# Performance work log

Measured on AMD Instinct MI355X. Metric: run time of the kernel, lower is better.

The kernel has to match this reference:

```python
import jax, jax.numpy as jnp
import numpy as np

NUM_MATCHES = 10
ALPHA = 0.75
INV_COEFF = 25.0
VAR_COEFF = 15.0
COV_COEFF = 1.0
GAMMA = 1.0


def cdist(a, b):
    # Euclidean pairwise distances via the matmul form (as torch.cdist p=2 does).
    d2 = (jnp.sum(a * a, -1)[:, :, None] + jnp.sum(b * b, -1)[:, None, :]
          - 2.0 * jnp.einsum('bnd,bmd->bnm', a, b))
    return jnp.sqrt(jnp.maximum(d2, 0.0))


def nearest_neighbors(input_maps, candidate_maps, distances, k):
    # Indices are constants wrt grads in the original (topk values discarded).
    distances = jax.lax.stop_gradient(distances)
    nn_d = jnp.min(distances, axis=-1)       # [B, N] distance to closest candidate
    nn_i = jnp.argmin(distances, axis=-1)    # [B, N] index of closest candidate
    _, element_indices = jax.lax.top_k(-nn_d, k)  # k elements with smallest NN distance
    candidate_indices = jnp.take_along_axis(nn_i, element_indices, axis=-1)
    # FAITHFUL to the source: torch gather with index shape [B, k, 1] keeps ONLY
    # feature channel 0 -> filtered maps have shape [B, k, 1].
    fi = jnp.take_along_axis(input_maps[:, :, :1], element_indices[:, :, None], axis=1)
    fc = jnp.take_along_axis(candidate_maps[:, :, :1], candidate_indices[:, :, None], axis=1)
    return fi, fc


def local_variance_loss(x, gamma):
    x = x - jnp.mean(x, axis=1, keepdims=True)
    std = jnp.sqrt(jnp.var(x, axis=1, ddof=1))  # torch std: unbiased
    return jnp.mean(jax.nn.relu(gamma - std))


def local_covariance_loss(x):
    B, N, D = x.shape
    x = x - jnp.mean(x, axis=1, keepdims=True)
    cov = jnp.einsum('bnd,bne->bde', x, x) / (N - 1)
    off_diag = 1.0 - jnp.eye(D, dtype=x.dtype)
    return jnp.sum((cov * off_diag) ** 2) / (D * B)


def local_vicreg_loss(x, y):
    inv = INV_COEFF * jnp.mean((x - y) ** 2)
    var = VAR_COEFF * (local_variance_loss(x, GAMMA) + local_variance_loss(y, GAMMA)) / 2
    cov = COV_COEFF * (local_covariance_loss(x) + local_covariance_loss(y)) / 2
    return inv, var, cov, inv + var + cov


def global_vicreg_loss(x, y):
    inv = INV_COEFF * jnp.mean((x - y) ** 2)

    def var_loss(z):
        std = jnp.sqrt(jnp.var(z, axis=0, ddof=1))
        return jnp.mean(jax.nn.relu(GAMMA - std))

    def cov_loss(z):
        n, d = z.shape
        z = z - jnp.mean(z, axis=0)
        cov = (z.T @ z) / (n - 1)
        off = 1.0 - jnp.eye(d, dtype=z.dtype)
        return jnp.sum((cov * off) ** 2) / d

    var = VAR_COEFF * (var_loss(x) + var_loss(y)) / 2
    cov = COV_COEFF * (cov_loss(x) + cov_loss(y)) / 2
    return inv, var, cov, inv + var + cov


def vicregl_forward(x1_maps, x2_maps, x1_glob, x2_glob, x1_locations, x2_locations):
    g = global_vicreg_loss(x1_glob, x2_glob)

    def location_loss(im, cm, il, cl):
        fi, fc = nearest_neighbors(im, cm, cdist(il, cl), NUM_MATCHES)
        return local_vicreg_loss(fi, fc)

    def feature_loss(im, cm):
        fi, fc = nearest_neighbors(im, cm, cdist(im, cm), NUM_MATCHES)
        return local_vicreg_loss(fi, fc)

    l1 = location_loss(x1_maps, x2_maps, x1_locations, x2_locations)
    l2 = location_loss(x2_maps, x1_maps, x2_locations, x1_locations)
    loc = tuple((a + b) / 2 for a, b in zip(l1, l2))

    f1 = feature_loss(x1_maps, x2_maps)
    f2 = feature_loss(x2_maps, x1_maps)
    feat = tuple((a + b) / 2 for a, b in zip(f1, f2))

    total = ALPHA * g[3] + (1.0 - ALPHA) * (feat[3] + loc[3]) / 2
    # Order: loss, global/(inv,var,cov,loss), location/(...), feature/(...)
    return jnp.stack([total, *g, *loc, *feat])


def setup_inputs() -> dict:
    key = jax.random.key(0)
    ks = jax.random.split(key, 6)
    B, N, D, G = 64, 1024, 512, 8192
    return {
        'x1_maps': jax.random.normal(ks[0], (B, N, D), jnp.float32),
        'x2_maps': jax.random.normal(ks[1], (B, N, D), jnp.float32),
        'x1_glob': jax.random.normal(ks[2], (B, G), jnp.float32),
        'x2_glob': jax.random.normal(ks[3], (B, G), jnp.float32),
        'x1_locations': jax.random.uniform(ks[4], (B, N, 2), jnp.float32),
        'x2_locations': jax.random.uniform(ks[5], (B, N, 2), jnp.float32),
    }


def reference(x1_maps, x2_maps, x1_glob, x2_glob, x1_locations, x2_locations):
    return vicregl_forward(x1_maps, x2_maps, x1_glob, x2_glob, x1_locations, x2_locations)
```

## Files before the change

kernel.cpp:

```cpp
#include <hip/hip_runtime.h>
#include <math.h>

#define NB 64
#define NN 1024
#define ND 512
#define NG 8192
#define FINF __builtin_inff()

typedef unsigned short u16;
typedef unsigned int   u32;
typedef short  short8 __attribute__((ext_vector_type(8)));
typedef float  f32x4  __attribute__((ext_vector_type(4)));

static const size_t OFF_AHL = 0;
static const size_t OFF_BHL = 33554432ull;
static const size_t PBASE_FAST = 67108864ull;

static const size_t OFF_FRPV = 0;
static const size_t OFF_FRPI = 524288;
static const size_t OFF_FCPV = 1048576;
static const size_t OFF_FCPI = 1572864;
static const size_t OFF_FRV  = 2097152;
static const size_t OFF_FRI  = 2162688;
static const size_t OFF_FCV  = 2228224;
static const size_t OFF_FCI  = 2293760;
static const size_t OFF_LRV  = 2359296;
static const size_t OFF_LRI  = 2424832;
static const size_t OFF_LCV  = 2490368;
static const size_t OFF_LCI  = 2555904;
static const size_t OFF_GP   = 2621440;
static const size_t OFF_SCAL = 3670016;
static const size_t OFF_SEL  = 3671056;
static const size_t OFF_RA   = 3676176;
static const size_t OFF_RB   = 3741712;
static const size_t OFF_GRED = 3807248;
static const size_t PBLOCK_END = 3807312;

__device__ __forceinline__ void upd(float& bv, int& bi, float v, int i){
  if (v < bv || (v == bv && i < bi)) { bv = v; bi = i; }
}

__device__ __forceinline__ u16 f2bf(float x){
  u32 u = __float_as_uint(x);
  u32 r = u + 0x7FFFu + ((u >> 16) & 1u);
  return (u16)(r >> 16);
}
__device__ __forceinline__ float bf2f(u16 h){ return __uint_as_float(((u32)h) << 16); }

__global__ __launch_bounds__(256) void convert_kernel(
    const float* __restrict__ X, u16* __restrict__ HL, float* __restrict__ norms)
{
  const int wid = threadIdx.x >> 6, lane = threadIdx.x & 63;
  const size_t row = (size_t)blockIdx.x * 4 + wid;
  const float* src = X + row * ND + lane * 8;
  float4 v0 = *(const float4*)src;
  float4 v1 = *(const float4*)(src + 4);
  float xs[8] = {v0.x, v0.y, v0.z, v0.w, v1.x, v1.y, v1.z, v1.w};
  short8 hi, lo;
  float nrm = 0.f;
  #pragma unroll
  for (int k = 0; k < 8; k++){
    u16 h = f2bf(xs[k]);
    float hf = bf2f(h);
    u16 l = f2bf(xs[k] - hf);
    hi[k] = (short)h; lo[k] = (short)l;
    nrm = fmaf(xs[k], xs[k], nrm);
  }
  #pragma unroll
  for (int off = 1; off < 64; off <<= 1) nrm += __shfl_xor(nrm, off);
  *(short8*)(HL + row * 1024 + lane * 8)       = hi;
  *(short8*)(HL + row * 1024 + 512 + lane * 8) = lo;
  if (lane == 0) norms[row] = nrm;
}

__device__ __forceinline__ int akoff(int s){ int p = s >> 3; return ((p == 2) ? 512 : 0) + (s & 7) * 64; }
__device__ __forceinline__ int bkoff(int s){ int p = s >> 3; return ((p == 1) ? 512 : 0) + (s & 7) * 64; }

__global__ __launch_bounds__(256) void feat_mfma_kernel(
    const u16* __restrict__ Ahl, const u16* __restrict__ Bhl,
    const float* __restrict__ ran, const float* __restrict__ rbn,
    float* __restrict__ rp_v, int* __restrict__ rp_i,
    float* __restrict__ cp_v, int* __restrict__ cp_i)
{
  const int blk = blockIdx.x;
  const int wg  = (blk & 7) * 512 + (blk >> 3);
  const int b = wg >> 6, t64 = wg & 63;
  const int ns = t64 >> 3, mt = t64 & 7;

  __shared__ u16 As[128 * 64];
  __shared__ u16 Bs[128 * 64];
  __shared__ float ra_s[128], rb_s[128];
  __shared__ float rowv[2][128]; __shared__ int rowi[2][128];
  __shared__ float colv[2][128]; __shared__ int coli[2][128];

  const int t = threadIdx.x;
  const int lane = t & 63, wid = t >> 6;
  const int wr = wid >> 1, wc = wid & 1;
  const int R0 = wr * 64, C0 = wc * 64;
  const int g4 = lane >> 4, l15 = lane & 15, swz = lane & 7;

  const u16* Agrow = Ahl + ((size_t)b * 1024 + ns * 128) * 1024;
  const u16* Bgrow = Bhl + ((size_t)b * 1024 + mt * 128) * 1024;

  if (t < 128) ra_s[t]       = ran[(size_t)b * 1024 + ns * 128 + t];
  else         rb_s[t - 128] = rbn[(size_t)b * 1024 + mt * 128 + (t - 128)];

  f32x4 acc[4][4];
  #pragma unroll
  for (int i = 0; i < 4; i++)
    #pragma unroll
    for (int j = 0; j < 4; j++){ f32x4 z = {0.f, 0.f, 0.f, 0.f}; acc[i][j] = z; }

  auto stage = [&](const u16* grow, u16* lds, int koff){
    #pragma unroll
    for (int i2 = 0; i2 < 4; i2++){
      int c = i2 * 256 + t;
      int row = c >> 3, col16 = c & 7;
      int srcc = col16 ^ (row & 7);
      const u16* g = grow + (size_t)row * 1024 + koff + srcc * 8;
      __builtin_amdgcn_global_load_lds(
          (const __attribute__((address_space(1))) void*)g,
          (__attribute__((address_space(3))) void*)(lds + c * 8),
          16, 0, 0);
    }
  };

  stage(Agrow, As, akoff(0));
  stage(Bgrow, Bs, bkoff(0));

  for (int s = 0; s < 24; s++){
    __syncthreads();
    #pragma unroll
    for (int kk = 0; kk < 64; kk += 32){
      short8 af[4], bfv[4];
      #pragma unroll
      for (int i2 = 0; i2 < 4; i2++){
        int ac16 = ((kk >> 3) + g4) ^ swz;
        int ar = R0 + i2 * 16 + l15;
        af[i2]  = *(const short8*)&As[ar * 64 + ac16 * 8];
        int br = C0 + i2 * 16 + l15;
        bfv[i2] = *(const short8*)&Bs[br * 64 + ac16 * 8];
      }
      #pragma unroll
      for (int i2 = 0; i2 < 4; i2++)
        #pragma unroll
        for (int j2 = 0; j2 < 4; j2++)
          acc[i2][j2] = __builtin_amdgcn_mfma_f32_16x16x32_bf16(af[i2], bfv[j2], acc[i2][j2], 0, 0, 0);
    }
    __syncthreads();
    if (s < 23){
      stage(Agrow, As, akoff(s + 1));
      stage(Bgrow, Bs, bkoff(s + 1));
    }
  }

  #pragma unroll
  for (int i2 = 0; i2 < 4; i2++){
    #pragma unroll
    for (int reg = 0; reg < 4; reg++){
      int rloc = R0 + i2 * 16 + g4 * 4 + reg;
      float rav = ra_s[rloc];
      float bv = FINF; int bi = 0;
      #pragma unroll
      for (int j2 = 0; j2 < 4; j2++){
        float d2 = rav + rb_s[C0 + j2 * 16 + l15] - 2.f * acc[i2][j2][reg];
        upd(bv, bi, d2, mt * 128 + C0 + j2 * 16 + l15);
      }
      #pragma unroll
      for (int off = 1; off < 16; off <<= 1){
        float ov = __shfl_xor(bv, off);
        int   oi = __shfl_xor(bi, off);
        upd(bv, bi, ov, oi);
      }
      if (l15 == 0){ rowv[wc][rloc] = bv; rowi[wc][rloc] = bi; }
    }
  }
  #pragma unroll
  for (int j2 = 0; j2 < 4; j2++){
    int cloc = C0 + j2 * 16 + l15;
    float rbv = rb_s[cloc];
    float bv = FINF; int bi = 0;
    #pragma unroll
    for (int i2 = 0; i2 < 4; i2++)
      #pragma unroll
      for (int reg = 0; reg < 4; reg++){
        float d2 = ra_s[R0 + i2 * 16 + g4 * 4 + reg] + rbv - 2.f * acc[i2][j2][reg];
        upd(bv, bi, d2, ns * 128 + R0 + i2 * 16 + g4 * 4 + reg);
      }
    #pragma unroll
    for (int off = 16; off < 64; off <<= 1){
      float ov = __shfl_xor(bv, off);
      int   oi = __shfl_xor(bi, off);
      upd(bv, bi, ov, oi);
    }
    if (g4 == 0){ colv[wr][cloc] = bv; coli[wr][cloc] = bi; }
  }
  __syncthreads();
  if (t < 128){
    float bv = rowv[0][t]; int bi = rowi[0][t];
    upd(bv, bi, rowv[1][t], rowi[1][t]);
    size_t o = ((size_t)b * 8 + mt) * NN + ns * 128 + t;
    rp_v[o] = bv; rp_i[o] = bi;
  } else {
    int c2 = t - 128;
    float bv = colv[0][c2]; int bi = coli[0][c2];
    upd(bv, bi, colv[1][c2], coli[1][c2]);
    size_t o = ((size_t)b * 8 + ns) * NN + mt * 128 + c2;
    cp_v[o] = bv; cp_i[o] = bi;
  }
}

__global__ __launch_bounds__(256) void feat_tile_kernel(
    const float* __restrict__ A, const float* __restrict__ Bm,
    float* __restrict__ rp_v, int* __restrict__ rp_i,
    float* __restrict__ cp_v, int* __restrict__ cp_i)
{
  const int blk = blockIdx.x;
  const int mt = blk & 7, ns = (blk >> 3) & 7, b = blk >> 6;
  const float* __restrict__ Ab = A  + ((size_t)b*NN + ns*128)*ND;
  const float* __restrict__ Bb = Bm + ((size_t)b*NN + mt*128)*ND;

  __shared__ __align__(16) float As[32*132];
  __shared__ __align__(16) float Bs[32*132];
  __shared__ float rasum[128], rbsum[128];
  __shared__ float colv[16*128];
  __shared__ int   coli[16*128];

  const int t = threadIdx.x;
  const int tx = t & 15, ty = t >> 4;

  float acc[8][8];
  #pragma unroll
  for (int i=0;i<8;i++)
    #pragma unroll
    for (int j=0;j<8;j++) acc[i][j]=0.f;
  float ra_acc=0.f, rb_acc=0.f;

  for (int kt=0; kt<ND; kt+=32){
    #pragma unroll
    for (int i=0;i<4;i++){
      int q = t + i*256;
      int r = q >> 3, f4 = q & 7;
      const float4 av  = *(const float4*)(Ab + (size_t)r*ND + kt + f4*4);
      const float4 bv4 = *(const float4*)(Bb + (size_t)r*ND + kt + f4*4);
      int kk = f4*4;
      As[(kk+0)*132+r]=av.x;  As[(kk+1)*132+r]=av.y;  As[(kk+2)*132+r]=av.z;  As[(kk+3)*132+r]=av.w;
      Bs[(kk+0)*132+r]=bv4.x; Bs[(kk+1)*132+r]=bv4.y; Bs[(kk+2)*132+r]=bv4.z; Bs[(kk+3)*132+r]=bv4.w;
    }
    __syncthreads();
    if (t < 128){
      #pragma unroll
      for (int kk=0;kk<32;kk++){ float v=As[kk*132+t]; ra_acc = fmaf(v,v,ra_acc); }
    } else {
      int c = t-128;
      #pragma unroll
      for (int kk=0;kk<32;kk++){ float v=Bs[kk*132+c]; rb_acc = fmaf(v,v,rb_acc); }
    }
    #pragma unroll
    for (int kk=0;kk<32;kk++){
      float a0[8], b0[8];
      *(float4*)&a0[0] = *(const float4*)&As[kk*132 + ty*8];
      *(float4*)&a0[4] = *(const float4*)&As[kk*132 + ty*8 + 4];
      *(float4*)&b0[0] = *(const float4*)&Bs[kk*132 + tx*8];
      *(float4*)&b0[4] = *(const float4*)&Bs[kk*132 + tx*8 + 4];
      #pragma unroll
      for (int i=0;i<8;i++)
        #pragma unroll
        for (int j=0;j<8;j++)
          acc[i][j] = fmaf(a0[i], b0[j], acc[i][j]);
    }
    __syncthreads();
  }

  if (t<128) rasum[t]=ra_acc; else rbsum[t-128]=rb_acc;
  __syncthreads();

  float ra[8], rb[8];
  #pragma unroll
  for (int i=0;i<8;i++){ ra[i]=rasum[ty*8+i]; rb[i]=rbsum[tx*8+i]; }

  const int n0g = ns*128, m0g = mt*128;

  #pragma unroll
  for (int i=0;i<8;i++){
    float bv = FINF; int bi = 0;
    #pragma unroll
    for (int j=0;j<8;j++){
      float d2 = ra[i] + rb[j] - 2.f*acc[i][j];
      upd(bv, bi, d2, m0g + tx*8 + j);
    }
    #pragma unroll
    for (int off=1; off<16; off<<=1){
      float ov = __shfl_xor(bv, off);
      int   oi = __shfl_xor(bi, off);
      upd(bv, bi, ov, oi);
    }
    if (tx==0){
      size_t o = ((size_t)b*8 + mt)*NN + n0g + ty*8 + i;
      rp_v[o] = bv; rp_i[o] = bi;
    }
  }
  #pragma unroll
  for (int j=0;j<8;j++){
    float bv = FINF; int bi = 0;
    #pragma unroll
    for (int i=0;i<8;i++){
      float d2 = ra[i] + rb[j] - 2.f*acc[i][j];
      upd(bv, bi, d2, n0g + ty*8 + i);
    }
    colv[ty*128 + tx*8 + j] = bv;
    coli[ty*128 + tx*8 + j] = bi;
  }
  __syncthreads();
  if (t < 128){
    float bv = FINF; int bi = 0;
    for (int y2=0;y2<16;y2++) upd(bv, bi, colv[y2*128+t], coli[y2*128+t]);
    size_t o = ((size_t)b*8 + ns)*NN + m0g + t;
    cp_v[o]=bv; cp_i[o]=bi;
  }
}

__global__ __launch_bounds__(256) void merge_kernel(
    const float* __restrict__ rp_v, const int* __restrict__ rp_i,
    const float* __restrict__ cp_v, const int* __restrict__ cp_i,
    float* __restrict__ row_v, int* __restrict__ row_i,
    float* __restrict__ col_v, int* __restrict__ col_i)
{
  int tid = blockIdx.x*256 + threadIdx.x;
  int which = tid >> 16;
  int r = tid & 65535;
  int b = r >> 10, n = r & 1023;
  float bv = FINF; int bi = 0;
  if (which == 0){
    #pragma unroll
    for (int p=0;p<8;p++){
      size_t o = ((size_t)b*8+p)*NN + n;
      upd(bv,bi, rp_v[o], rp_i[o]);
    }
    row_v[(size_t)b*NN+n]=bv; row_i[(size_t)b*NN+n]=bi;
  } else {
    #pragma unroll
    for (int p=0;p<8;p++){
      size_t o = ((size_t)b*8+p)*NN + n;
      upd(bv,bi, cp_v[o], cp_i[o]);
    }
    col_v[(size_t)b*NN+n]=bv; col_i[(size_t)b*NN+n]=bi;
  }
}

__global__ __launch_bounds__(256) void loc_kernel(
    const float* __restrict__ L1, const float* __restrict__ L2,
    float* __restrict__ lr_v, int* __restrict__ lr_i,
    float* __restrict__ lc_v, int* __restrict__ lc_i)
{
  int b = blockIdx.x >> 2, part = blockIdx.x & 3, t = threadIdx.x;
  __shared__ float2 p1[NN], p2[NN];
  for (int i=t;i<NN;i+=256){
    p1[i] = ((const float2*)L1)[(size_t)b*NN+i];
    p2[i] = ((const float2*)L2)[(size_t)b*NN+i];
  }
  __syncthreads();
  int n = part*256 + t;
  {
    float2 a = p1[n];
    float bv=FINF; int bi=0;
    for (int m=0;m<NN;m++){
      float dx=a.x-p2[m].x, dy=a.y-p2[m].y;
      float d2 = dx*dx+dy*dy;
      if (d2 < bv){ bv=d2; bi=m; }
    }
    lr_v[(size_t)b*NN+n]=bv; lr_i[(size_t)b*NN+n]=bi;
  }
  {
    float2 a = p2[n];
    float bv=FINF; int bi=0;
    for (int q=0;q<NN;q++){
      float dx=a.x-p1[q].x, dy=a.y-p1[q].y;
      float d2 = dx*dx+dy*dy;
      if (d2 < bv){ bv=d2; bi=q; }
    }
    lc_v[(size_t)b*NN+n]=bv; lc_i[(size_t)b*NN+n]=bi;
  }
}

__global__ __launch_bounds__(256) void glob_part_kernel(
    const float* __restrict__ X, const float* __restrict__ Y,
    float* __restrict__ Gpart, float* __restrict__ scalpart)
{
  int blk = blockIdx.x, t = threadIdx.x;
  int d0 = blk*64;
  __shared__ float xt[64*65];
  __shared__ float yt[64*65];
  __shared__ float red[256];

  float inv_part = 0.f;
  #pragma unroll
  for (int i=0;i<16;i++){
    int q = t + i*256;
    int n = q>>6, c = q&63;
    float xv = X[(size_t)n*NG + d0 + c];
    float yv = Y[(size_t)n*NG + d0 + c];
    xt[n*65+c]=xv; yt[n*65+c]=yv;
    float df = xv-yv; inv_part += df*df;
  }
  __syncthreads();

  float relu_part=0.f, csq2_part=0.f;
  if (t < 128){
    int c = t & 63;
    float* Z = (t<64)? xt : yt;
    float s=0.f;
    for (int n=0;n<64;n++) s += Z[n*65+c];
    float mu = s*(1.f/64.f);
    float sq=0.f;
    for (int n=0;n<64;n++){ float v=Z[n*65+c]-mu; Z[n*65+c]=v; sq = fmaf(v,v,sq); }
    float sd = sqrtf(sq*(1.f/63.f));
    relu_part = fmaxf(0.f, 1.f-sd);
    csq2_part = sq*sq;
  }
  __syncthreads();

  int ti=(t>>4)*4, tj=(t&15)*4;
  for (int pass=0; pass<2; pass++){
    const float* Z = pass? yt : xt;
    float g[4][4] = {};
    for (int c=0;c<64;c++){
      float vi[4], vj[4];
      #pragma unroll
      for (int k2=0;k2<4;k2++){ vi[k2]=Z[(ti+k2)*65+c]; vj[k2]=Z[(tj+k2)*65+c]; }
      #pragma unroll
      for (int a2=0;a2<4;a2++)
        #pragma unroll
        for (int b2=0;b2<4;b2++) g[a2][b2] = fmaf(vi[a2], vj[b2], g[a2][b2]);
    }
    float* gp = Gpart + ((size_t)blk*2+pass)*4096;
    #pragma unroll
    for (int a2=0;a2<4;a2++)
      #pragma unroll
      for (int b2=0;b2<4;b2++) gp[(ti+a2)*64 + tj + b2] = g[a2][b2];
  }

  auto bsum = [&](float v)->float{
    red[t]=v; __syncthreads();
    for (int s=128;s;s>>=1){ if (t<s) red[t]+=red[t+s]; __syncthreads(); }
    float r=red[0]; __syncthreads(); return r;
  };
  float inv_s = bsum(inv_part);
  float rx_s  = bsum(t<64 ? relu_part : 0.f);
  float ry_s  = bsum((t>=64 && t<128)? relu_part : 0.f);
  float cx_s  = bsum(t<64 ? csq2_part : 0.f);
  float cy_s  = bsum((t>=64 && t<128)? csq2_part : 0.f);
  if (t==0){
    float* sp = scalpart + blk*8;
    sp[0]=inv_s; sp[1]=rx_s; sp[2]=ry_s; sp[3]=cx_s; sp[4]=cy_s;
  }
}

__global__ __launch_bounds__(256) void glob_reduce2_kernel(
    const float* __restrict__ Gpart, float* __restrict__ gred)
{
  int g = blockIdx.x, t = threadIdx.x;
  __shared__ float red[256];
  int pass = t >> 7, e = g*128 + (t & 127);
  float s = 0.f;
  for (int blk=0; blk<128; blk++) s += Gpart[((size_t)blk*2 + pass)*4096 + e];
  red[t] = s*s; __syncthreads();
  for (int st=64; st; st>>=1){ if ((t&127) < st) red[t] += red[t+st]; __syncthreads(); }
  if ((t&127)==0) gred[g*2 + pass] = red[t];
}

__global__ __launch_bounds__(64) void select_kernel(
    const float* __restrict__ x1m, const float* __restrict__ x2m,
    const float* __restrict__ frv, const int* __restrict__ fri,
    const float* __restrict__ fcv, const int* __restrict__ fci,
    const float* __restrict__ lrv, const int* __restrict__ lri,
    const float* __restrict__ lcv, const int* __restrict__ lci,
    float* __restrict__ selout)
{
  int sel = blockIdx.x >> 6, b = blockIdx.x & 63;
  const float* nnv; const int* nni; const float* inm; const float* cnm;
  if      (sel==0){ nnv=frv; nni=fri; inm=x1m; cnm=x2m; }
  else if (sel==1){ nnv=fcv; nni=fci; inm=x2m; cnm=x1m; }
  else if (sel==2){ nnv=lrv; nni=lri; inm=x1m; cnm=x2m; }
  else            { nnv=lcv; nni=lci; inm=x2m; cnm=x1m; }

  int lane = threadIdx.x;
  float v[16];
  #pragma unroll
  for (int j=0;j<16;j++) v[j] = nnv[(size_t)b*NN + j*64 + lane];
  __shared__ int wins[10];
  for (int it=0; it<10; it++){
    float bv = FINF; int bi = 0x7fffffff;
    #pragma unroll
    for (int j=0;j<16;j++) upd(bv, bi, v[j], j*64+lane);
    #pragma unroll
    for (int off=1; off<64; off<<=1){
      float ov = __shfl_xor(bv, off);
      int   oi = __shfl_xor(bi, off);
      upd(bv, bi, ov, oi);
    }
    #pragma unroll
    for (int j=0;j<16;j++) if (j*64+lane == bi) v[j] = FINF;
    if (lane==0) wins[it] = bi;
  }
  __syncthreads();
  if (lane < 10){
    int e = wins[lane];
    int c = nni[(size_t)b*NN + e];
    float fi = inm[((size_t)b*NN + e)*ND];
    float fc = cnm[((size_t)b*NN + c)*ND];
    float2* so = (float2*)selout;
    so[((size_t)sel*64 + b)*10 + lane] = make_float2(fi, fc);
  }
}

__global__ __launch_bounds__(64) void final_kernel(
    const float* __restrict__ selout, const float* __restrict__ gred,
    const float* __restrict__ scalpart, float* __restrict__ out)
{
  int lane = threadIdx.x;
  float ssx = (lane<32)? gred[lane*2]   : 0.f;
  float ssy = (lane<32)? gred[lane*2+1] : 0.f;
  const float* sp0 = scalpart + (size_t)lane*8;
  const float* sp1 = scalpart + (size_t)(lane+64)*8;
  float inv_p = sp0[0]+sp1[0];
  float rx = sp0[1]+sp1[1], ry = sp0[2]+sp1[2];
  float cx = sp0[3]+sp1[3], cy = sp0[4]+sp1[4];
  #pragma unroll
  for (int off=1; off<64; off<<=1){
    ssx += __shfl_xor(ssx,off); ssy += __shfl_xor(ssy,off);
    inv_p += __shfl_xor(inv_p,off);
    rx += __shfl_xor(rx,off); ry += __shfl_xor(ry,off);
    cx += __shfl_xor(cx,off); cy += __shfl_xor(cy,off);
  }

  float inv_s[4], var_s[4];
  #pragma unroll
  for (int sel=0; sel<4; sel++){
    const float2* so = (const float2*)selout + ((size_t)sel*64 + lane)*10;
    float x[10], y[10];
    float sx=0.f, sy=0.f, sd2=0.f;
    #pragma unroll
    for (int j=0;j<10;j++){
      float2 p = so[j];
      x[j]=p.x; y[j]=p.y;
      sx+=p.x; sy+=p.y;
      float d=p.x-p.y; sd2 = fmaf(d,d,sd2);
    }
    float mx = sx*0.1f, my = sy*0.1f;
    float vx=0.f, vy=0.f;
    #pragma unroll
    for (int j=0;j<10;j++){
      float dx=x[j]-mx, dy=y[j]-my;
      vx = fmaf(dx,dx,vx); vy = fmaf(dy,dy,vy);
    }
    vx *= (1.f/9.f); vy *= (1.f/9.f);
    float rvx = fmaxf(0.f, 1.f - sqrtf(vx));
    float rvy = fmaxf(0.f, 1.f - sqrtf(vy));
    float a=sd2, b2=rvx, c=rvy;
    #pragma unroll
    for (int off=32; off; off>>=1){
      a  += __shfl_xor(a, off);
      b2 += __shfl_xor(b2, off);
      c  += __shfl_xor(c, off);
    }
    inv_s[sel] = 25.f * a * (1.f/640.f);
    var_s[sel] = 15.f*0.5f*(b2*(1.f/64.f) + c*(1.f/64.f));
  }
  if (lane==0){
    float g_inv = 25.f * inv_p / (64.f*8192.f);
    float g_var = 15.f*0.5f*((rx+ry)*(1.f/8192.f));
    float covx = (ssx - cx)/(63.f*63.f*8192.f);
    float covy = (ssy - cy)/(63.f*63.f*8192.f);
    float g_cov = 0.5f*(covx+covy);
    float g_loss = g_inv+g_var+g_cov;
    float feat_inv=0.5f*(inv_s[0]+inv_s[1]);
    float feat_var=0.5f*(var_s[0]+var_s[1]);
    float feat_loss=feat_inv+feat_var;
    float loc_inv=0.5f*(inv_s[2]+inv_s[3]);
    float loc_var=0.5f*(var_s[2]+var_s[3]);
    float loc_loss=loc_inv+loc_var;
    float total = 0.75f*g_loss + 0.25f*0.5f*(feat_loss+loc_loss);
    out[0]=total;
    out[1]=g_inv;   out[2]=g_var;   out[3]=g_cov; out[4]=g_loss;
    out[5]=loc_inv; out[6]=loc_var; out[7]=0.f;   out[8]=loc_loss;
    out[9]=feat_inv;out[10]=feat_var;out[11]=0.f; out[12]=feat_loss;
  }
}

extern "C" void kernel_launch(void* const* d_in, const int* in_sizes, int n_in,
                              void* d_out, int out_size, void* d_ws, size_t ws_size,
                              hipStream_t stream)
{
  const float* x1m = (const float*)d_in[0];
  const float* x2m = (const float*)d_in[1];
  const float* x1g = (const float*)d_in[2];
  const float* x2g = (const float*)d_in[3];
  const float* x1l = (const float*)d_in[4];
  const float* x2l = (const float*)d_in[5];
  float* out = (float*)d_out;
  float* w = (float*)d_ws;

  const size_t need_fast = (PBASE_FAST + PBLOCK_END) * 4ull;
  const bool fast = (ws_size >= need_fast);
  const size_t pb = fast ? PBASE_FAST : 0;

  u16* Ahl = (u16*)(w + OFF_AHL);
  u16* Bhl = (u16*)(w + OFF_BHL);
  float* frpv = w + pb + OFF_FRPV;  int* frpi = (int*)(w + pb + OFF_FRPI);
  float* fcpv = w + pb + OFF_FCPV;  int* fcpi = (int*)(w + pb + OFF_FCPI);
  float* frv  = w + pb + OFF_FRV;   int* fri  = (int*)(w + pb + OFF_FRI);
  float* fcv  = w + pb + OFF_FCV;   int* fci  = (int*)(w + pb + OFF_FCI);
  float* lrv  = w + pb + OFF_LRV;   int* lri  = (int*)(w + pb + OFF_LRI);
  float* lcv  = w + pb + OFF_LCV;   int* lci  = (int*)(w + pb + OFF_LCI);
  float* gp   = w + pb + OFF_GP;
  float* scal = w + pb + OFF_SCAL;
  float* selw = w + pb + OFF_SEL;
  float* ra   = w + pb + OFF_RA;
  float* rb   = w + pb + OFF_RB;
  float* gred = w + pb + OFF_GRED;

  if (fast){
    convert_kernel<<<dim3(16384), dim3(256), 0, stream>>>(x1m, Ahl, ra);
    convert_kernel<<<dim3(16384), dim3(256), 0, stream>>>(x2m, Bhl, rb);
    feat_mfma_kernel<<<dim3(4096), dim3(256), 0, stream>>>(Ahl, Bhl, ra, rb,
                                                           frpv, frpi, fcpv, fcpi);
  } else {
    feat_tile_kernel<<<dim3(4096), dim3(256), 0, stream>>>(x1m, x2m, frpv, frpi, fcpv, fcpi);
  }

  merge_kernel<<<dim3(512), dim3(256), 0, stream>>>(frpv, frpi, fcpv, fcpi,
                                                    frv, fri, fcv, fci);

  glob_part_kernel<<<dim3(128), dim3(256), 0, stream>>>(x1g, x2g, gp, scal);
  glob_reduce2_kernel<<<dim3(32), dim3(256), 0, stream>>>(gp, gred);

  loc_kernel<<<dim3(256), dim3(256), 0, stream>>>(x1l, x2l, lrv, lri, lcv, lci);

  select_kernel<<<dim3(256), dim3(64), 0, stream>>>(x1m, x2m, frv, fri, fcv, fci,
                                                    lrv, lri, lcv, lci, selw);
  final_kernel<<<dim3(1), dim3(64), 0, stream>>>(selw, gred, scal, out);
}
```

Measured before the change: 750.0 us.

## Double-buffer LDS tiles in feature MFMA kernel with prefetch two stages ahead

Converts the single-buffered A/B LDS staging in the distance MFMA kernel into a double-buffered pipeline. Loads for stage s+2 are issued right after stage s's compute, and partial vmcnt waits replace full syncthreads, so global-to-LDS traffic overlaps MFMA work. It also raises wave priority around the MFMA block. The cost is doubled LDS use (32KB for tiles), which may lower occupancy, and the manual waitcnt/barrier logic is fragile.

```diff
diff --git a/kernel.cpp b/kernel.cpp
--- a/kernel.cpp
+++ b/kernel.cpp
@@ -87,8 +87,8 @@
   const int b = wg >> 6, t64 = wg & 63;
   const int ns = t64 >> 3, mt = t64 & 7;
 
-  __shared__ u16 As[128 * 64];
-  __shared__ u16 Bs[128 * 64];
+  __shared__ u16 As[2][128 * 64];
+  __shared__ u16 Bs[2][128 * 64];
   __shared__ float ra_s[128], rb_s[128];
   __shared__ float rowv[2][128]; __shared__ int rowi[2][128];
   __shared__ float colv[2][128]; __shared__ int coli[2][128];
@@ -111,25 +111,43 @@
     #pragma unroll
     for (int j = 0; j < 4; j++){ f32x4 z = {0.f, 0.f, 0.f, 0.f}; acc[i][j] = z; }
 
-  auto stage = [&](const u16* grow, u16* lds, int koff){
+  auto stageAB = [&](int buf, int s){
+    const int ka = akoff(s), kb = bkoff(s);
+    u16* la = &As[buf][0];
+    u16* lb = &Bs[buf][0];
     #pragma unroll
     for (int i2 = 0; i2 < 4; i2++){
       int c = i2 * 256 + t;
       int row = c >> 3, col16 = c & 7;
       int srcc = col16 ^ (row & 7);
-      const u16* g = grow + (size_t)row * 1024 + koff + srcc * 8;
       __builtin_amdgcn_global_load_lds(
-          (const __attribute__((address_space(1))) void*)g,
-          (__attribute__((address_space(3))) void*)(lds + c * 8),
-          16, 0, 0);
+          (const __attribute__((address_space(1))) void*)(Agrow + (size_t)row * 1024 + ka + srcc * 8),
+          (__attribute__((address_space(3))) void*)(la + c * 8), 16, 0, 0);
+    }
+    #pragma unroll
+    for (int i2 = 0; i2 < 4; i2++){
+      int c = i2 * 256 + t;
+      int row = c >> 3, col16 = c & 7;
+      int srcc = col16 ^ (row & 7);
+      __builtin_amdgcn_global_load_lds(
+          (const __attribute__((address_space(1))) void*)(Bgrow + (size_t)row * 1024 + kb + srcc * 8),
+          (__attribute__((address_space(3))) void*)(lb + c * 8), 16, 0, 0);
     }
   };
 
-  stage(Agrow, As, akoff(0));
-  stage(Bgrow, Bs, bkoff(0));
-
+  stageAB(0, 0);
+  stageAB(1, 1);
+
+  int cur = 0;
   for (int s = 0; s < 24; s++){
-    __syncthreads();
+    if (s == 23) asm volatile("s_waitcnt vmcnt(0)" ::: "memory");
+    else         asm volatile("s_waitcnt vmcnt(8)" ::: "memory");
+    __builtin_amdgcn_s_barrier();
+    __builtin_amdgcn_sched_barrier(0);
+
+    const u16* Asb = &As[cur][0];
+    const u16* Bsb = &Bs[cur][0];
+    __builtin_amdgcn_s_setprio(1);
     #pragma unroll
     for (int kk = 0; kk < 64; kk += 32){
       short8 af[4], bfv[4];
@@ -137,9 +155,9 @@
       for (int i2 = 0; i2 < 4; i2++){
         int ac16 = ((kk >> 3) + g4) ^ swz;
         int ar = R0 + i2 * 16 + l15;
-        af[i2]  = *(const short8*)&As[ar * 64 + ac16 * 8];
+        af[i2]  = *(const short8*)&Asb[ar * 64 + ac16 * 8];
         int br = C0 + i2 * 16 + l15;
-        bfv[i2] = *(const short8*)&Bs[br * 64 + ac16 * 8];
+        bfv[i2] = *(const short8*)&Bsb[br * 64 + ac16 * 8];
       }
       #pragma unroll
       for (int i2 = 0; i2 < 4; i2++)
@@ -147,11 +165,12 @@
         for (int j2 = 0; j2 < 4; j2++)
           acc[i2][j2] = __builtin_amdgcn_mfma_f32_16x16x32_bf16(af[i2], bfv[j2], acc[i2][j2], 0, 0, 0);
     }
-    __syncthreads();
-    if (s < 23){
-      stage(Agrow, As, akoff(s + 1));
-      stage(Bgrow, Bs, bkoff(s + 1));
-    }
+    __builtin_amdgcn_s_setprio(0);
+    __builtin_amdgcn_sched_barrier(0);
+    __builtin_amdgcn_s_barrier();
+    __builtin_amdgcn_sched_barrier(0);
+    if (s < 22) stageAB(cur, s + 2);
+    cur ^= 1;
   }
 
   #pragma unroll
```

After: 766.9 us. 2.3% more time.
